# Optimization experiments

Measured on AMD Instinct MI355X. Metric: run time of the kernel, lower is better.

Reference implementation:

```python
import jax, jax.numpy as jnp
import numpy as np

EMBED_DIM = 768
NUM_HEADS = 12
HEAD_DIM = EMBED_DIM // NUM_HEADS


def setup_inputs() -> dict:
    key = jax.random.key(0)
    k_x, k_qkv, k_w, k_b = jax.random.split(key, 4)
    B, N, D = 1, 4096, EMBED_DIM
    scale = 1.0 / np.sqrt(D)
    x = jax.random.normal(k_x, (B, N, D), dtype=jnp.float32)
    # nn.Linear weights: stored as [out, in]; we apply x @ W.T
    w_qkv = jax.random.normal(k_qkv, (3 * D, D), dtype=jnp.float32) * scale
    w_out = jax.random.normal(k_w, (D, D), dtype=jnp.float32) * scale
    b_out = jax.random.normal(k_b, (D,), dtype=jnp.float32) * 0.01
    return {"x": x, "w_qkv": w_qkv, "w_out": w_out, "b_out": b_out}


def reference(x, w_qkv, w_out, b_out):
    B, N, D = x.shape
    H, Hd = NUM_HEADS, HEAD_DIM
    qkv = (x @ w_qkv.T).reshape(B, N, 3, H, Hd)
    q, k, v = qkv[:, :, 0], qkv[:, :, 1], qkv[:, :, 2]
    scores = jnp.einsum('bnhd,bmhd->bhnm', q, k) / jnp.sqrt(jnp.float32(Hd))
    attn = jax.nn.softmax(scores, axis=-1)
    out = jnp.einsum('bhnm,bmhd->bnhd', attn, v).reshape(B, N, D)
    return out @ w_out.T + b_out
```

## Files before the change

### kernel.cpp

```cpp
#include <hip/hip_runtime.h>


typedef __attribute__((ext_vector_type(8))) short short8;
typedef __attribute__((ext_vector_type(4))) float f32x4;

#define N_TOK 4096
#define NHEAD 12
#define DMODEL 768
#define QK_LD 1536

#if defined(__has_builtin)
#if __has_builtin(__builtin_amdgcn_exp2f)
#define EXP2F __builtin_amdgcn_exp2f
#else
#define EXP2F exp2f
#endif
#else
#define EXP2F exp2f
#endif

#if defined(__has_builtin)
#if __has_builtin(__builtin_amdgcn_perm)
#define PACK2BF(hi, lo) __builtin_amdgcn_perm((hi), (lo), 0x07060302u)
#else
#define PACK2BF(hi, lo) ((((hi)) & 0xffff0000u) | (((lo)) >> 16))
#endif
#else
#define PACK2BF(hi, lo) ((((hi)) & 0xffff0000u) | (((lo)) >> 16))
#endif

__device__ __forceinline__ ushort bf16bits(float x) {
  union { float f; unsigned u; } cv; cv.f = x;
  unsigned u = cv.u;
  u += 0x7fffu + ((u >> 16) & 1u);
  return (ushort)(u >> 16);
}
__device__ __forceinline__ float bf2f(ushort u) {
  return __uint_as_float(((unsigned)u) << 16);
}

__device__ __forceinline__ void async16(ushort* lds, const ushort* g) {
  __builtin_amdgcn_global_load_lds((const __attribute__((address_space(1))) unsigned int*)g,
                                   (__attribute__((address_space(3))) unsigned int*)lds,
                                   16, 0, 0);
}

__global__ void __launch_bounds__(256) cvt3(const float* __restrict__ x,
                                            const float* __restrict__ wq,
                                            const float* __restrict__ wo,
                                            ushort* __restrict__ xb,
                                            ushort* __restrict__ wqb,
                                            ushort* __restrict__ wob) {
  const int b = blockIdx.x, t = threadIdx.x;
  const float* src; ushort* dst; int i;
  if (b < 3072)      { src = x;  dst = xb;  i = b * 256 + t; }
  else if (b < 4800) { src = wq; dst = wqb; i = (b - 3072) * 256 + t; }
  else               { src = wo; dst = wob; i = (b - 4800) * 256 + t; }
  const float4 v = ((const float4*)src)[i];
  ushort4 o;
  o.x = bf16bits(v.x); o.y = bf16bits(v.y); o.z = bf16bits(v.z); o.w = bf16bits(v.w);
  ((ushort4*)dst)[i] = o;
}

#define GEMM_STAGE(Ms, Mp, MK)                                                 \
  do {                                                                         \
    _Pragma("unroll")                                                          \
    for (int i_ = 0; i_ < 4; i_++)                                             \
      async16(&Ms[(wave * 32 + i_ * 8) * 64],                                  \
              Mp + (size_t)(wave * 32 + i_ * 8 + lrow) * (MK) + lcol);         \
  } while (0)

#define GEMM_STAGE96(Ms, Mp, MK)                                               \
  do {                                                                         \
    _Pragma("unroll")                                                          \
    for (int i_ = 0; i_ < 3; i_++)                                             \
      async16(&Ms[(wave * 24 + i_ * 8) * 64],                                  \
              Mp + (size_t)(wave * 24 + i_ * 8 + lrow) * (MK) + lcol);         \
  } while (0)

#define GEMM_STAGE64(Ms, Mp, MK)                                               \
  do {                                                                         \
    _Pragma("unroll")                                                          \
    for (int i_ = 0; i_ < 2; i_++)                                             \
      async16(&Ms[(wave * 16 + i_ * 8) * 64],                                  \
              Mp + (size_t)(wave * 16 + i_ * 8 + lrow) * (MK) + lcol);         \
  } while (0)

__global__ void __launch_bounds__(256) gemm_qkv(const ushort* __restrict__ A,
                                                const ushort* __restrict__ B,
                                                ushort* __restrict__ qkb,
                                                ushort* __restrict__ vtg) {
  __shared__ __align__(16) ushort As[128 * 64];
  __shared__ __align__(16) ushort Bs[96 * 64];
  const int tid = threadIdx.x;
  const int wave = tid >> 6, lane = tid & 63, quad = lane >> 4, l16 = lane & 15;
  const int wm = wave & 1, wn = wave >> 1;
  const int lrow = lane >> 3, lcol = (lane & 7) * 8;
  const int m0 = blockIdx.y * 128, n0 = blockIdx.x * 96;
  const int K = DMODEL;

  f32x4 acc[4][3] = {};
  const ushort* Ap = A + (size_t)m0 * K;
  const ushort* Bp = B + (size_t)n0 * K;

  for (int k0 = 0; k0 < K; k0 += 64) {
    GEMM_STAGE(As, Ap + k0, K);
    GEMM_STAGE96(Bs, Bp + k0, K);
    __syncthreads();
#pragma unroll
    for (int ks = 0; ks < 2; ks++) {
      short8 af[4], bf[3];
#pragma unroll
      for (int i = 0; i < 4; i++)
        af[i] = *(const short8*)&As[(wm * 64 + i * 16 + l16) * 64 + ks * 32 + quad * 8];
#pragma unroll
      for (int i = 0; i < 3; i++)
        bf[i] = *(const short8*)&Bs[(wn * 48 + i * 16 + l16) * 64 + ks * 32 + quad * 8];
#pragma unroll
      for (int mi = 0; mi < 4; mi++)
#pragma unroll
        for (int ni = 0; ni < 3; ni++)
          acc[mi][ni] = __builtin_amdgcn_mfma_f32_16x16x32_bf16(af[mi], bf[ni], acc[mi][ni], 0, 0, 0);
    }
    __syncthreads();
  }

  if (n0 < QK_LD) {
    const float qsc = (n0 < 768) ? 0.18033688011112042f : 1.0f;
#pragma unroll
    for (int mi = 0; mi < 4; mi++)
#pragma unroll
      for (int ni = 0; ni < 3; ni++) {
        const int col = n0 + wn * 48 + ni * 16 + l16;
#pragma unroll
        for (int rr = 0; rr < 4; rr++) {
          const int row = m0 + wm * 64 + mi * 16 + quad * 4 + rr;
          qkb[(size_t)row * QK_LD + col] = bf16bits(acc[mi][ni][rr] * qsc);
        }
      }
  } else {
#pragma unroll
    for (int mi = 0; mi < 4; mi++)
#pragma unroll
      for (int ni = 0; ni < 3; ni++) {
        const int col = n0 + wn * 48 + ni * 16 + l16 - QK_LD;
        const int rowb = m0 + wm * 64 + mi * 16 + quad * 4;
        const unsigned u0 = (unsigned)bf16bits(acc[mi][ni][0]) |
                            ((unsigned)bf16bits(acc[mi][ni][1]) << 16);
        const unsigned u1 = (unsigned)bf16bits(acc[mi][ni][2]) |
                            ((unsigned)bf16bits(acc[mi][ni][3]) << 16);
        *(uint2*)&vtg[(size_t)col * N_TOK + rowb] = make_uint2(u0, u1);
      }
  }
}

__global__ void __launch_bounds__(256) gemm_out(const ushort* __restrict__ A,
                                                const ushort* __restrict__ B,
                                                float* __restrict__ Cf,
                                                const float* __restrict__ bias) {
  __shared__ __align__(16) ushort As[64 * 64];
  __shared__ __align__(16) ushort Bs[64 * 64];
  const int tid = threadIdx.x;
  const int wave = tid >> 6, lane = tid & 63, quad = lane >> 4, l16 = lane & 15;
  const int wm = wave & 1, wn = wave >> 1;
  const int lrow = lane >> 3, lcol = (lane & 7) * 8;
  const int m0 = blockIdx.y * 64, n0 = blockIdx.x * 64;
  const int K = DMODEL, Nn = DMODEL;

  f32x4 acc[2][2] = {};
  const ushort* Ap = A + (size_t)m0 * K;
  const ushort* Bp = B + (size_t)n0 * K;

  for (int k0 = 0; k0 < K; k0 += 64) {
    GEMM_STAGE64(As, Ap + k0, K);
    GEMM_STAGE64(Bs, Bp + k0, K);
    __syncthreads();
#pragma unroll
    for (int ks = 0; ks < 2; ks++) {
      short8 af[2], bf[2];
#pragma unroll
      for (int i = 0; i < 2; i++) {
        af[i] = *(const short8*)&As[(wm * 32 + i * 16 + l16) * 64 + ks * 32 + quad * 8];
        bf[i] = *(const short8*)&Bs[(wn * 32 + i * 16 + l16) * 64 + ks * 32 + quad * 8];
      }
#pragma unroll
      for (int mi = 0; mi < 2; mi++)
#pragma unroll
        for (int ni = 0; ni < 2; ni++)
          acc[mi][ni] = __builtin_amdgcn_mfma_f32_16x16x32_bf16(af[mi], bf[ni], acc[mi][ni], 0, 0, 0);
    }
    __syncthreads();
  }

#pragma unroll
  for (int mi = 0; mi < 2; mi++)
#pragma unroll
    for (int ni = 0; ni < 2; ni++) {
      const int col = n0 + wn * 32 + ni * 16 + l16;
#pragma unroll
      for (int rr = 0; rr < 4; rr++) {
        const int row = m0 + wm * 32 + mi * 16 + quad * 4 + rr;
        Cf[(size_t)row * Nn + col] = acc[mi][ni][rr] + bias[col];
      }
    }
}


#define ATTN_STAGE(bufi)                                                       \
  do {                                                                         \
    async16(&Ks[bufi][(wave * 16) * 64],     kp0);                             \
    async16(&Ks[bufi][(wave * 16 + 8) * 64], kp1);                             \
    async16(&Vs[bufi][(wave * 16) * 64],     vp0);                             \
    async16(&Vs[bufi][(wave * 16 + 8) * 64], vp1);                             \
    kp0 += (size_t)64 * QK_LD; kp1 += (size_t)64 * QK_LD;                      \
    vp0 += 64; vp1 += 64;                                                      \
  } while (0)

#define WAITBAR4()                                                             \
  do {                                                                         \
    asm volatile("s_waitcnt vmcnt(4) lgkmcnt(0)" ::: "memory");                \
    __builtin_amdgcn_s_barrier();                                              \
  } while (0)

#define WAITBAR0()                                                             \
  do {                                                                         \
    asm volatile("s_waitcnt vmcnt(0) lgkmcnt(0)" ::: "memory");                \
    __builtin_amdgcn_s_barrier();                                              \
  } while (0)

#define ATTN_TILE(KbP, VbP)                                                    \
  do {                                                                         \
    const ushort* Kb_ = (KbP);                                                 \
    const ushort* Vb_ = (VbP);                                                 \
    _Pragma("unroll")                                                          \
    for (int ks = 0; ks < 2; ks++) {                                           \
      union { unsigned u[4]; short8 v; } pfu0, pfu1;                           \
      _Pragma("unroll")                                                        \
      for (int h2 = 0; h2 < 2; h2++) {                                         \
        const int nt = 2 * ks + h2;                                            \
        const short8 kf0 = *(const short8*)&Kb_[(nt * 16 + l16) * 64 + u0];    \
        const short8 kf1 = *(const short8*)&Kb_[(nt * 16 + l16) * 64 + u1];    \
        f32x4 a0 = __builtin_amdgcn_mfma_f32_16x16x32_bf16(kf0, qf[0][0], z4, 0, 0, 0); \
        a0 = __builtin_amdgcn_mfma_f32_16x16x32_bf16(kf1, qf[0][1], a0, 0, 0, 0);       \
        f32x4 a1 = __builtin_amdgcn_mfma_f32_16x16x32_bf16(kf0, qf[1][0], z4, 0, 0, 0); \
        a1 = __builtin_amdgcn_mfma_f32_16x16x32_bf16(kf1, qf[1][1], a1, 0, 0, 0);       \
        {                                                                      \
          const float e0 = EXP2F(a0[0]);                                       \
          const float e1 = EXP2F(a0[1]);                                       \
          const float e2 = EXP2F(a0[2]);                                       \
          const float e3 = EXP2F(a0[3]);                                       \
          lsum[0] += (e0 + e1) + (e2 + e3);                                    \
          pfu0.u[2 * h2]     = PACK2BF(__float_as_uint(e1), __float_as_uint(e0)); \
          pfu0.u[2 * h2 + 1] = PACK2BF(__float_as_uint(e3), __float_as_uint(e2)); \
        }                                                                      \
        {                                                                      \
          const float e0 = EXP2F(a1[0]);                                       \
          const float e1 = EXP2F(a1[1]);                                       \
          const float e2 = EXP2F(a1[2]);                                       \
          const float e3 = EXP2F(a1[3]);                                       \
          lsum[1] += (e0 + e1) + (e2 + e3);                                    \
          pfu1.u[2 * h2]     = PACK2BF(__float_as_uint(e1), __float_as_uint(e0)); \
          pfu1.u[2 * h2 + 1] = PACK2BF(__float_as_uint(e3), __float_as_uint(e2)); \
        }                                                                      \
      }                                                                        \
      const short8 pf0 = pfu0.v, pf1 = pfu1.v;                                 \
      _Pragma("unroll")                                                        \
      for (int dt = 0; dt < 4; dt++) {                                         \
        const short8 vf = *(const short8*)&Vb_[(dt * 16 + l16) * 64 + (ks ? u1 : u0)]; \
        o[0][dt] = __builtin_amdgcn_mfma_f32_16x16x32_bf16(pf0, vf, o[0][dt], 0, 0, 0); \
        o[1][dt] = __builtin_amdgcn_mfma_f32_16x16x32_bf16(pf1, vf, o[1][dt], 0, 0, 0); \
      }                                                                        \
    }                                                                          \
  } while (0)

__global__ void __launch_bounds__(256, 3) attn_flash(const ushort* __restrict__ qk,
                                                     const ushort* __restrict__ vtg,
                                                     ushort* __restrict__ pob,
                                                     float* __restrict__ pl,
                                                     int ntiles, int nsl8) {
  __shared__ __align__(16) ushort Ks[3][64 * 64];
  __shared__ __align__(16) ushort Vs[3][64 * 64];

  const int b = blockIdx.x;
  const int s8 = b & 7;
  const int j = b >> 3;
  const int slice = s8 + 8 * (j % nsl8);
  const int qb = j / nsl8;
  const int h = slice % NHEAD;
  const int sp = slice / NHEAD;

  const int tid = threadIdx.x;
  const int wave = tid >> 6, lane = tid & 63, quad = lane >> 4, l16 = lane & 15;
  const int q0 = qb * 128 + wave * 32;

  short8 qf[2][2];
#pragma unroll
  for (int s = 0; s < 2; s++) {
    const ushort* qp = qk + (size_t)(q0 + s * 16 + l16) * QK_LD + h * 64 + quad * 8;
    qf[s][0] = *(const short8*)qp;
    qf[s][1] = *(const short8*)(qp + 32);
  }

  const int srow = wave * 16 + (lane >> 3);
  const int un = (((lane & 7) ^ (lane >> 3)) * 8);
  const int g0 = ((srow >> 5) << 5) + (((srow >> 2) & 3) << 3) +
                 (((srow >> 4) & 1) << 2) + (srow & 3);
  const int kt0 = sp * ntiles;
  const ushort* kp0 = qk + 768 + h * 64 + un + (size_t)(kt0 * 64 + g0) * QK_LD;
  const ushort* kp1 = kp0 + (size_t)16 * QK_LD;
  const ushort* vp0 = vtg + (size_t)(h * 64 + srow) * N_TOK + kt0 * 64 + un;
  const ushort* vp1 = vp0 + (size_t)8 * N_TOK;

  const int u0 = (quad ^ (l16 & 7)) * 8;
  const int u1 = u0 ^ 32;

  f32x4 o[2][4] = {};
  float lsum[2] = {};
  const f32x4 z4 = {};

  ATTN_STAGE(0);
  ATTN_STAGE(1);
  WAITBAR4();

  int bc = 0;
  int bs = 2;
  for (int kt = 0; kt < ntiles; kt++) {
    const bool more = (kt + 2 < ntiles);
    if (more) ATTN_STAGE(bs);
    ATTN_TILE(Ks[bc], Vs[bc]);
    if (more) WAITBAR4(); else WAITBAR0();
    bc = (bc == 2) ? 0 : bc + 1;
    bs = (bs == 2) ? 0 : bs + 1;
  }

#pragma unroll
  for (int s = 0; s < 2; s++) {
    float lt = lsum[s];
    lt += __shfl_xor(lt, 16, 64);
    lt += __shfl_xor(lt, 32, 64);
#pragma unroll
    for (int rr = 0; rr < 4; rr++) {
      const float l = __shfl(lt, quad * 16 + quad * 4 + rr, 64);
      const float inv = 1.f / l;
      const int row = q0 + s * 16 + quad * 4 + rr;
      if (l16 == 0)
        pl[(size_t)(sp * NHEAD + h) * N_TOK + row] = l;
#pragma unroll
      for (int dt = 0; dt < 4; dt++)
        pob[((size_t)sp * N_TOK + row) * DMODEL + h * 64 + dt * 16 + l16] =
            bf16bits(o[s][dt][rr] * inv);
    }
  }
}

__global__ void __launch_bounds__(256) combine(const ushort* __restrict__ pob,
                                               const float* __restrict__ pl,
                                               ushort* __restrict__ aout, int S) {
  const int i = blockIdx.x * 256 + threadIdx.x;
  const int row = i / (DMODEL / 4);
  const int hd = (i % (DMODEL / 4)) * 4;
  const int h = hd >> 6;
  float lt = 0.f, a0 = 0.f, a1 = 0.f, a2 = 0.f, a3 = 0.f;
  for (int s = 0; s < S; s++) {
    const float l = pl[((size_t)s * NHEAD + h) * N_TOK + row];
    const ushort4 a = *(const ushort4*)&pob[((size_t)s * N_TOK + row) * DMODEL + hd];
    lt += l;
    a0 += l * bf2f(a.x); a1 += l * bf2f(a.y); a2 += l * bf2f(a.z); a3 += l * bf2f(a.w);
  }
  const float inv = 1.f / lt;
  ushort4 r;
  r.x = bf16bits(a0 * inv); r.y = bf16bits(a1 * inv);
  r.z = bf16bits(a2 * inv); r.w = bf16bits(a3 * inv);
  *(ushort4*)&aout[(size_t)row * DMODEL + hd] = r;
}

extern "C" void kernel_launch(void* const* d_in, const int* in_sizes, int n_in,
                              void* d_out, int out_size, void* d_ws, size_t ws_size,
                              hipStream_t stream) {
  const float* x     = (const float*)d_in[0];
  const float* w_qkv = (const float*)d_in[1];
  const float* w_out = (const float*)d_in[2];
  const float* b_out = (const float*)d_in[3];
  float* out = (float*)d_out;

  const size_t PO_UNIT = 6291456UL;
  const int S = (ws_size >= 4 * PO_UNIT + 20840448UL) ? 4 : 2;
  char* ws = (char*)d_ws;
  ushort* pob   = (ushort*)ws;
  ushort* xb    = (ushort*)ws;
  ushort* wqkvb = (ushort*)(ws + 6291456UL);
  ushort* qkb   = (ushort*)(ws + (size_t)S * PO_UNIT);
  ushort* vtg   = (ushort*)((char*)qkb + 12582912UL);
  ushort* woutb = (ushort*)((char*)vtg + 6291456UL);
  float*  pl    = (float*)((char*)woutb + 1179648UL);
  ushort* aoutb = qkb;

  cvt3<<<5376, 256, 0, stream>>>(x, w_qkv, w_out, xb, wqkvb, woutb);

  gemm_qkv<<<dim3(24, 32), 256, 0, stream>>>(xb, wqkvb, qkb, vtg);

  attn_flash<<<384 * S, 256, 0, stream>>>(qkb, vtg, pob, pl, 64 / S, (12 * S) / 8);

  combine<<<3072, 256, 0, stream>>>(pob, pl, aoutb, S);

  gemm_out<<<dim3(12, 64), 256, 0, stream>>>(aoutb, woutb, out, b_out);
}
```

Measured before the change: 187.1 us.

## Double-buffer LDS tiles in both GEMMs and halve QKV GEMM M tile

```diff
diff --git a/kernel.cpp b/kernel.cpp
--- a/kernel.cpp
+++ b/kernel.cpp
@@ -62,19 +62,11 @@
   ((ushort4*)dst)[i] = o;
 }
 
-#define GEMM_STAGE(Ms, Mp, MK)                                                 \
-  do {                                                                         \
-    _Pragma("unroll")                                                          \
-    for (int i_ = 0; i_ < 4; i_++)                                             \
-      async16(&Ms[(wave * 32 + i_ * 8) * 64],                                  \
-              Mp + (size_t)(wave * 32 + i_ * 8 + lrow) * (MK) + lcol);         \
-  } while (0)
-
 #define GEMM_STAGE96(Ms, Mp, MK)                                               \
   do {                                                                         \
     _Pragma("unroll")                                                          \
     for (int i_ = 0; i_ < 3; i_++)                                             \
-      async16(&Ms[(wave * 24 + i_ * 8) * 64],                                  \
+      async16(&(Ms)[(wave * 24 + i_ * 8) * 64],                                \
               Mp + (size_t)(wave * 24 + i_ * 8 + lrow) * (MK) + lcol);         \
   } while (0)
 
@@ -82,7 +74,7 @@
   do {                                                                         \
     _Pragma("unroll")                                                          \
     for (int i_ = 0; i_ < 2; i_++)                                             \
-      async16(&Ms[(wave * 16 + i_ * 8) * 64],                                  \
+      async16(&(Ms)[(wave * 16 + i_ * 8) * 64],                                \
               Mp + (size_t)(wave * 16 + i_ * 8 + lrow) * (MK) + lcol);         \
   } while (0)
 
@@ -90,34 +82,40 @@
                                                 const ushort* __restrict__ B,
                                                 ushort* __restrict__ qkb,
                                                 ushort* __restrict__ vtg) {
-  __shared__ __align__(16) ushort As[128 * 64];
-  __shared__ __align__(16) ushort Bs[96 * 64];
+  __shared__ __align__(16) ushort As[2][64 * 64];
+  __shared__ __align__(16) ushort Bs[2][96 * 64];
   const int tid = threadIdx.x;
   const int wave = tid >> 6, lane = tid & 63, quad = lane >> 4, l16 = lane & 15;
   const int wm = wave & 1, wn = wave >> 1;
   const int lrow = lane >> 3, lcol = (lane & 7) * 8;
-  const int m0 = blockIdx.y * 128, n0 = blockIdx.x * 96;
+  const int m0 = blockIdx.y * 64, n0 = blockIdx.x * 96;
   const int K = DMODEL;
 
-  f32x4 acc[4][3] = {};
+  f32x4 acc[2][3] = {};
   const ushort* Ap = A + (size_t)m0 * K;
   const ushort* Bp = B + (size_t)n0 * K;
 
+  GEMM_STAGE64(As[0], Ap, K);
+  GEMM_STAGE96(Bs[0], Bp, K);
+  __syncthreads();
+
   for (int k0 = 0; k0 < K; k0 += 64) {
-    GEMM_STAGE(As, Ap + k0, K);
-    GEMM_STAGE96(Bs, Bp + k0, K);
-    __syncthreads();
+    const int cur = (k0 >> 6) & 1, nxt = cur ^ 1;
+    if (k0 + 64 < K) {
+      GEMM_STAGE64(As[nxt], Ap + k0 + 64, K);
+      GEMM_STAGE96(Bs[nxt], Bp + k0 + 64, K);
+    }
 #pragma unroll
     for (int ks = 0; ks < 2; ks++) {
-      short8 af[4], bf[3];
-#pragma unroll
-      for (int i = 0; i < 4; i++)
-        af[i] = *(const short8*)&As[(wm * 64 + i * 16 + l16) * 64 + ks * 32 + quad * 8];
+      short8 af[2], bf[3];
+#pragma unroll
+      for (int i = 0; i < 2; i++)
+        af[i] = *(const short8*)&As[cur][(wm * 32 + i * 16 + l16) * 64 + ks * 32 + quad * 8];
 #pragma unroll
       for (int i = 0; i < 3; i++)
-        bf[i] = *(const short8*)&Bs[(wn * 48 + i * 16 + l16) * 64 + ks * 32 + quad * 8];
-#pragma unroll
-      for (int mi = 0; mi < 4; mi++)
+        bf[i] = *(const short8*)&Bs[cur][(wn * 48 + i * 16 + l16) * 64 + ks * 32 + quad * 8];
+#pragma unroll
+      for (int mi = 0; mi < 2; mi++)
 #pragma unroll
         for (int ni = 0; ni < 3; ni++)
           acc[mi][ni] = __builtin_amdgcn_mfma_f32_16x16x32_bf16(af[mi], bf[ni], acc[mi][ni], 0, 0, 0);
@@ -128,23 +126,23 @@
   if (n0 < QK_LD) {
     const float qsc = (n0 < 768) ? 0.18033688011112042f : 1.0f;
 #pragma unroll
-    for (int mi = 0; mi < 4; mi++)
+    for (int mi = 0; mi < 2; mi++)
 #pragma unroll
       for (int ni = 0; ni < 3; ni++) {
         const int col = n0 + wn * 48 + ni * 16 + l16;
 #pragma unroll
         for (int rr = 0; rr < 4; rr++) {
-          const int row = m0 + wm * 64 + mi * 16 + quad * 4 + rr;
+          const int row = m0 + wm * 32 + mi * 16 + quad * 4 + rr;
           qkb[(size_t)row * QK_LD + col] = bf16bits(acc[mi][ni][rr] * qsc);
         }
       }
   } else {
 #pragma unroll
-    for (int mi = 0; mi < 4; mi++)
+    for (int mi = 0; mi < 2; mi++)
 #pragma unroll
       for (int ni = 0; ni < 3; ni++) {
         const int col = n0 + wn * 48 + ni * 16 + l16 - QK_LD;
-        const int rowb = m0 + wm * 64 + mi * 16 + quad * 4;
+        const int rowb = m0 + wm * 32 + mi * 16 + quad * 4;
         const unsigned u0 = (unsigned)bf16bits(acc[mi][ni][0]) |
                             ((unsigned)bf16bits(acc[mi][ni][1]) << 16);
         const unsigned u1 = (unsigned)bf16bits(acc[mi][ni][2]) |
@@ -158,8 +156,8 @@
                                                 const ushort* __restrict__ B,
                                                 float* __restrict__ Cf,
                                                 const float* __restrict__ bias) {
-  __shared__ __align__(16) ushort As[64 * 64];
-  __shared__ __align__(16) ushort Bs[64 * 64];
+  __shared__ __align__(16) ushort As[2][64 * 64];
+  __shared__ __align__(16) ushort Bs[2][64 * 64];
   const int tid = threadIdx.x;
   const int wave = tid >> 6, lane = tid & 63, quad = lane >> 4, l16 = lane & 15;
   const int wm = wave & 1, wn = wave >> 1;
@@ -171,17 +169,23 @@
   const ushort* Ap = A + (size_t)m0 * K;
   const ushort* Bp = B + (size_t)n0 * K;
 
+  GEMM_STAGE64(As[0], Ap, K);
+  GEMM_STAGE64(Bs[0], Bp, K);
+  __syncthreads();
+
   for (int k0 = 0; k0 < K; k0 += 64) {
-    GEMM_STAGE64(As, Ap + k0, K);
-    GEMM_STAGE64(Bs, Bp + k0, K);
-    __syncthreads();
+    const int cur = (k0 >> 6) & 1, nxt = cur ^ 1;
+    if (k0 + 64 < K) {
+      GEMM_STAGE64(As[nxt], Ap + k0 + 64, K);
+      GEMM_STAGE64(Bs[nxt], Bp + k0 + 64, K);
+    }
 #pragma unroll
     for (int ks = 0; ks < 2; ks++) {
       short8 af[2], bf[2];
 #pragma unroll
       for (int i = 0; i < 2; i++) {
-        af[i] = *(const short8*)&As[(wm * 32 + i * 16 + l16) * 64 + ks * 32 + quad * 8];
-        bf[i] = *(const short8*)&Bs[(wn * 32 + i * 16 + l16) * 64 + ks * 32 + quad * 8];
+        af[i] = *(const short8*)&As[cur][(wm * 32 + i * 16 + l16) * 64 + ks * 32 + quad * 8];
+        bf[i] = *(const short8*)&Bs[cur][(wn * 32 + i * 16 + l16) * 64 + ks * 32 + quad * 8];
       }
 #pragma unroll
       for (int mi = 0; mi < 2; mi++)
@@ -397,7 +401,7 @@
 
   cvt3<<<5376, 256, 0, stream>>>(x, w_qkv, w_out, xb, wqkvb, woutb);
 
-  gemm_qkv<<<dim3(24, 32), 256, 0, stream>>>(xb, wqkvb, qkb, vtg);
+  gemm_qkv<<<dim3(24, 64), 256, 0, stream>>>(xb, wqkvb, qkb, vtg);
 
   attn_flash<<<384 * S, 256, 0, stream>>>(qkb, vtg, pob, pl, 64 / S, (12 * S) / 8);
 
```

After: 186.1 us (median of 2 runs). Within noise of the previous version (-0.5%).
